# Optimization experiments

Hardware: AMD Instinct MI355X
Metric: run time of the kernel (lower is better)

The kernel has to match this reference:

```python
import jax, jax.numpy as jnp
import numpy as np

B = 512       # batch_size
IN = 256      # input_size
H = 512       # hidden_size
OUT = 64      # output_size
N_PAIRS = B - 1   # number of H0 persistence deaths (connected components merges)
TOL = 1e-6    # rtol for torch.isclose
ATOL = 1e-8   # torch default atol
EPS = 0.0     # homology_eps
TARGET_P = 1.0
HOM_P = 1.0
COMP_P = 0.01

_IU = np.triu_indices(B, 1)  # condensed pdist indexing, static


def _mlp(batch, W1, b1, W2, b2, W3, b3, Wout, bout):
    # FeedForward: input->hidden, (n_layers-1) hidden->hidden, hidden->output, ReLU
    h = jax.nn.relu(batch @ W1 + b1)
    h = jax.nn.relu(h @ W2 + b2)
    h = jax.nn.relu(h @ W3 + b3)
    return h @ Wout + bout


def _pdist(y):
    # condensed euclidean pairwise distances, same ordering as torch F.pdist
    d = y[_IU[0]] - y[_IU[1]]                 # [P, OUT]
    return jnp.sqrt(jnp.sum(d * d, axis=-1))  # [P]


def setup_inputs() -> dict:
    key = jax.random.key(0)
    ks = jax.random.split(key, 8)
    batch = jax.random.normal(ks[0], (B, IN), jnp.float32)
    target = jax.random.normal(ks[1], (B, OUT), jnp.float32)
    W1 = jax.random.normal(ks[2], (IN, H), jnp.float32) / np.sqrt(IN)
    W2 = jax.random.normal(ks[3], (H, H), jnp.float32) / np.sqrt(H)
    W3 = jax.random.normal(ks[4], (H, H), jnp.float32) / np.sqrt(H)
    Wout = jax.random.normal(ks[5], (H, OUT), jnp.float32) / np.sqrt(H)
    b1 = jnp.zeros((H,), jnp.float32)
    b2 = jnp.zeros((H,), jnp.float32)
    b3 = jnp.zeros((H,), jnp.float32)
    bout = jnp.zeros((OUT,), jnp.float32)
    # persistence deaths = actual critical pdist values (from the external
    # Vietoris-Rips routine in the original); sample N_PAIRS distinct entries.
    y0 = _mlp(batch, W1, b1, W2, b2, W3, b3, Wout, bout)
    pd0 = np.asarray(_pdist(y0))
    idx = np.random.default_rng(0).choice(pd0.shape[0], N_PAIRS, replace=False)
    persistence_deaths = jnp.asarray(pd0[idx], jnp.float32)
    return {"batch": batch, "target": target,
            "W1": W1, "b1": b1, "W2": W2, "b2": b2, "W3": W3, "b3": b3,
            "Wout": Wout, "bout": bout,
            "persistence_deaths": persistence_deaths}


def reference(batch, target, W1, b1, W2, b2, W3, b3, Wout, bout, persistence_deaths):
    y = _mlp(batch, W1, b1, W2, b2, W3, b3, Wout, bout)   # [B, OUT]
    y_hom = y  # normalize_for_homology = False
    pd = _pdist(y_hom)                                     # [P]
    # vectorized indicator_death over all pairs (replaces per-pair Python loop)
    mask = jnp.any(jnp.isclose(pd[:, None], persistence_deaths[None, :],
                               rtol=TOL, atol=ATOL), axis=1)      # [P] bool
    # homology_dim=0: birth_pdist = 0; norm=1 of selected (death - 0 + eps)
    homology_loss = jnp.sum(jnp.abs(jnp.where(mask, pd + EPS, 0.0)))
    target_loss = jnp.mean((target - y) ** 2)
    compactness_loss = jnp.sum(jnp.abs(y - jnp.mean(y, axis=0, keepdims=True)))
    loss = TARGET_P * target_loss + HOM_P * homology_loss + COMP_P * compactness_loss
    return loss
```

## Files before the change

kernel.cpp:

```cpp
#include <hip/hip_runtime.h>

#define B_    512
#define IN_   256
#define H_    512
#define OUT_  64
#define NDEATH (B_ - 1)
#define NSORT  512
#define RTOL_ 1e-6
#define ATOL_ 1e-8
#define NBLK  256
#define NTHR  512
#define KT    32

typedef __attribute__((ext_vector_type(4))) double d4_t;

__device__ __forceinline__ void ast(double* p, double v) {
    __hip_atomic_store(p, v, __ATOMIC_RELAXED, __HIP_MEMORY_SCOPE_AGENT);
}
__device__ __forceinline__ double ald(const double* p) {
    return __hip_atomic_load(p, __ATOMIC_RELAXED, __HIP_MEMORY_SCOPE_AGENT);
}

__device__ __forceinline__ void lbar() {
    asm volatile("s_waitcnt lgkmcnt(0)" ::: "memory");
    __builtin_amdgcn_s_barrier();
    asm volatile("" ::: "memory");
}

__device__ __forceinline__ void gbar(unsigned* cnt, unsigned nb) {
    __syncthreads();
    if (threadIdx.x == 0) {
        __hip_atomic_fetch_add(cnt, 1u, __ATOMIC_RELAXED,
                               __HIP_MEMORY_SCOPE_AGENT);
        while (__hip_atomic_load(cnt, __ATOMIC_RELAXED,
                                 __HIP_MEMORY_SCOPE_AGENT) < nb)
            __builtin_amdgcn_s_sleep(2);
    }
    __syncthreads();
}

__device__ void sort_windows(const float* __restrict__ deaths,
                             double* sd, double* slo, double* shi, int t) {
    if (t < NSORT) sd[t] = (t < NDEATH) ? (double)deaths[t] : 1e300;
    __syncthreads();
    for (int k = 2; k <= NSORT; k <<= 1) {
        for (int j = k >> 1; j > 0; j >>= 1) {
            if (t < 256) {
                int l = ((t & ~(j - 1)) << 1) | (t & (j - 1));
                int p = l + j;
                bool up = ((l & k) == 0);
                double a = sd[l], b = sd[p];
                if ((a > b) == up) { sd[l] = b; sd[p] = a; }
            }
            __syncthreads();
        }
    }
    if (t < NSORT) {
        double d = sd[t];
        double w = ATOL_ + RTOL_ * fabs(d);
        slo[t] = d - w;
        shi[t] = d + w;
    }
    __syncthreads();
}

template <typename TIN, bool RELU>
__device__ void gemm_dev(const TIN* __restrict__ A, const float* __restrict__ W,
                         const float* __restrict__ bias, double* __restrict__ C,
                         int N, int K, int tile, int t,
                         double (&As)[2][2][KT][33], double (&Ws)[2][2][KT][33]) {
    const int lane  = t & 63;
    const int wave4 = (t >> 6) & 3;
    const int w2    = t >> 8;
    const int tg    = t & 255;
    const int wm    = wave4 & 1, wn = wave4 >> 1;
    const int nbx   = N >> 5;
    const int row0  = (tile / nbx) << 5;
    const int col0  = (tile % nbx) << 5;

    const int akk   = tg & 31;
    const int amm   = tg >> 5;
    const int wnn   = tg & 31;
    const int wkk   = tg >> 5;
    const int kbase = w2 * (K >> 1);
    const int nkt   = K >> 6;

    TIN   ar[2][4];
    float wr[2][4];

    auto load_to = [&](int rs, int kt) {
        const int k0 = kbase + (kt << 5);
        #pragma unroll
        for (int p = 0; p < 4; ++p) {
            ar[rs][p] = A[(size_t)(row0 + amm + 8 * p) * K + k0 + akk];
            wr[rs][p] = W[(size_t)(k0 + wkk + 8 * p) * N + col0 + wnn];
        }
    };
    auto stage = [&](int rs, int buf) {
        #pragma unroll
        for (int p = 0; p < 4; ++p) {
            As[w2][buf][akk][amm + 8 * p] = (double)ar[rs][p];
            Ws[w2][buf][wkk + 8 * p][wnn] = (double)wr[rs][p];
        }
    };

    load_to(0, 0);
    if (nkt > 1) load_to(1, 1);
    stage(0, 0);
    lbar();

    d4_t c4 = {0.0, 0.0, 0.0, 0.0};
    const int mrow = wm * 16 + (lane & 15);
    const int ncol = wn * 16 + (lane & 15);
    const int kq   = lane >> 4;

    for (int kt = 0; kt < nkt; ++kt) {
        const int cur = kt & 1;
        if (kt + 2 < nkt) load_to(cur, kt + 2);
        #pragma unroll
        for (int ks = 0; ks < KT / 4; ++ks) {
            double av = As[w2][cur][ks * 4 + kq][mrow];
            double bv = Ws[w2][cur][ks * 4 + kq][ncol];
            c4 = __builtin_amdgcn_mfma_f64_16x16x4f64(av, bv, c4, 0, 0, 0);
        }
        if (kt + 1 < nkt) stage(cur ^ 1, cur ^ 1);
        lbar();
    }

    double (*cEx)[16][17] = (double (*)[16][17])(&As[0][0][0][0]);
    const int r4 = (lane >> 4) * 4;
    if (w2 == 1) {
        #pragma unroll
        for (int r = 0; r < 4; ++r)
            cEx[wave4][r4 + r][lane & 15] = c4[r];
    }
    lbar();
    if (w2 == 0) {
        #pragma unroll
        for (int r = 0; r < 4; ++r) {
            int row = row0 + wm * 16 + r4 + r;
            int col = col0 + wn * 16 + (lane & 15);
            double v = c4[r] + cEx[wave4][r4 + r][lane & 15] + (double)bias[col];
            if (RELU) v = v > 0.0 ? v : 0.0;
            ast(&C[(size_t)row * N + col], v);
        }
    }
}

__device__ void mc_dev(const float* __restrict__ target,
                       const double* __restrict__ y,
                       double* __restrict__ t_part, double* __restrict__ c_part,
                       int c, int t) {
    const int wave = t >> 6, lane = t & 63;
    double v = y[(size_t)t * OUT_ + c];
    double s = v;
    for (int off = 32; off; off >>= 1) s += __shfl_down(s, off);
    __shared__ double swm[8];
    __shared__ double smean;
    if (lane == 0) swm[wave] = s;
    __syncthreads();
    if (t == 0) {
        double m = 0.0;
        #pragma unroll
        for (int w = 0; w < 8; ++w) m += swm[w];
        smean = m / (double)B_;
    }
    __syncthreads();
    double m = smean;
    double d = (double)target[(size_t)t * OUT_ + c] - v;
    double t_s = d * d;
    double c_s = fabs(v - m);
    for (int off = 32; off; off >>= 1) {
        t_s += __shfl_down(t_s, off);
        c_s += __shfl_down(c_s, off);
    }
    __shared__ double st[8], sc[8];
    if (lane == 0) { st[wave] = t_s; sc[wave] = c_s; }
    __syncthreads();
    if (t == 0) {
        double ts = 0.0, cs = 0.0;
        #pragma unroll
        for (int w = 0; w < 8; ++w) { ts += st[w]; cs += sc[w]; }
        ast(&t_part[c], ts);
        ast(&c_part[c], cs);
    }
}

__device__ __forceinline__ double pair_val(const double* __restrict__ yrow_s,
                                           const double* __restrict__ yj,
                                           const double* __restrict__ slo,
                                           const double* __restrict__ shi) {
    double s = 0.0;
    #pragma unroll
    for (int d = 0; d < OUT_; d += 2) {
        double2 v = *(const double2*)(yj + d);
        double d0 = yrow_s[d]     - v.x;
        double d1 = yrow_s[d + 1] - v.y;
        s = fma(d0, d0, s);
        s = fma(d1, d1, s);
    }
    double pd = sqrt(s);
    int pos = 0;
    #pragma unroll
    for (int step = NSORT / 2; step; step >>= 1) {
        if (slo[pos + step - 1] <= pd) pos += step;
    }
    bool m = (pos > 0) && (shi[pos - 1] >= pd);
    return m ? pd : 0.0;
}

__device__ void pdist_dev(const double* __restrict__ y,
                          double* __restrict__ hom_part, int bid, int t,
                          double* yA, double* yB,
                          const double* slo, const double* shi) {
    const int iA = bid;
    const int iB = 510 - bid;
    if (t < OUT_)            yA[t]        = y[(size_t)iA * OUT_ + t];
    else if (t < 2 * OUT_)   yB[t - OUT_] = y[(size_t)iB * OUT_ + (t - OUT_)];
    __syncthreads();

    double local = 0.0;
    for (int j = iA + 1 + t; j < B_; j += NTHR)
        local += pair_val(yA, y + (size_t)j * OUT_, slo, shi);
    if (iB != iA)
        for (int j = iB + 1 + t; j < B_; j += NTHR)
            local += pair_val(yB, y + (size_t)j * OUT_, slo, shi);

    for (int off = 32; off; off >>= 1) local += __shfl_down(local, off);
    __shared__ double sw[8];
    int wave = t >> 6, lane = t & 63;
    if (lane == 0) sw[wave] = local;
    __syncthreads();
    if (t == 0) {
        double s = 0.0;
        #pragma unroll
        for (int w = 0; w < 8; ++w) s += sw[w];
        ast(&hom_part[bid], s);
    }
}

__global__ __launch_bounds__(NTHR) void fused_k(
    const float* __restrict__ batch, const float* __restrict__ target,
    const float* __restrict__ W1, const float* __restrict__ b1,
    const float* __restrict__ W2, const float* __restrict__ b2,
    const float* __restrict__ W3, const float* __restrict__ b3,
    const float* __restrict__ Wout, const float* __restrict__ bout,
    const float* __restrict__ deaths, float* __restrict__ out,
    double* __restrict__ hA, double* __restrict__ hB,
    double* __restrict__ hC, double* __restrict__ yv,
    double* __restrict__ hom_part, double* __restrict__ t_part,
    double* __restrict__ c_part, unsigned* __restrict__ cnt,
    double* __restrict__ wbc) {
    const int bid = blockIdx.x;
    const int t   = threadIdx.x;
    const int g   = bid >> 4;
    const int c   = bid & 15;
    unsigned* gc  = cnt + g * 32;

    __shared__ double As[2][2][KT][33];
    __shared__ double Ws[2][2][KT][33];
    __shared__ double slo[NSORT], shi[NSORT];
    __shared__ double yA[OUT_], yB[OUT_];
    __shared__ int    lastf;
    double* sd = &As[0][0][0][0];

    gemm_dev<float,  true>(batch, W1, b1, hA, H_, IN_, bid, t, As, Ws);
    gbar(&gc[0], 16);
    gemm_dev<double, true>(hA, W2, b2, hB, H_, H_, bid, t, As, Ws);
    gbar(&gc[1], 16);
    gemm_dev<double, true>(hB, W3, b3, hC, H_, H_, bid, t, As, Ws);
    gbar(&gc[2], 16);

    if (c < 2) {
        gemm_dev<double, false>(hC, Wout, bout, yv, OUT_, H_, g * 2 + c, t, As, Ws);
    } else {
        sort_windows(deaths, sd, slo, shi, t);
        if (bid == 2 && t < NSORT) {
            ast(&wbc[t],         slo[t]);
            ast(&wbc[NSORT + t], shi[t]);
        }
    }

    gbar(&cnt[512], NBLK);
    if (c < 2) {
        if (t < NSORT) {
            slo[t] = ald(&wbc[t]);
            shi[t] = ald(&wbc[NSORT + t]);
        }
        __syncthreads();
    }

    pdist_dev(yv, hom_part, bid, t, yA, yB, slo, shi);
    if (bid < OUT_) mc_dev(target, yv, t_part, c_part, bid, t);

    __syncthreads();
    if (t == 0) {
        unsigned prev = __hip_atomic_fetch_add(&cnt[544], 1u, __ATOMIC_RELAXED,
                                               __HIP_MEMORY_SCOPE_AGENT);
        lastf = (prev == NBLK - 1);
    }
    __syncthreads();
    if (lastf) {
        double h = 0.0, tp = 0.0, cp = 0.0;
        if (t < NBLK)
            h = __hip_atomic_load(&hom_part[t], __ATOMIC_RELAXED,
                                  __HIP_MEMORY_SCOPE_AGENT);
        if (t < OUT_) {
            tp = __hip_atomic_load(&t_part[t], __ATOMIC_RELAXED,
                                   __HIP_MEMORY_SCOPE_AGENT);
            cp = __hip_atomic_load(&c_part[t], __ATOMIC_RELAXED,
                                   __HIP_MEMORY_SCOPE_AGENT);
        }
        for (int off = 32; off; off >>= 1) {
            h  += __shfl_down(h,  off);
            tp += __shfl_down(tp, off);
            cp += __shfl_down(cp, off);
        }
        __shared__ double sh[8], stp[8], scp[8];
        int wave = t >> 6, lane = t & 63;
        if (lane == 0) { sh[wave] = h; stp[wave] = tp; scp[wave] = cp; }
        __syncthreads();
        if (t == 0) {
            double hs = 0.0, ts = 0.0, cs = 0.0;
            #pragma unroll
            for (int w = 0; w < 8; ++w) {
                hs += sh[w]; ts += stp[w]; cs += scp[w];
            }
            out[0] = (float)(ts / (double)(B_ * OUT_) + hs + 0.01 * cs);
        }
    }
}

extern "C" void kernel_launch(void* const* d_in, const int* in_sizes, int n_in,
                              void* d_out, int out_size, void* d_ws, size_t ws_size,
                              hipStream_t stream) {
    const float* batch  = (const float*)d_in[0];
    const float* target = (const float*)d_in[1];
    const float* W1     = (const float*)d_in[2];
    const float* b1     = (const float*)d_in[3];
    const float* W2     = (const float*)d_in[4];
    const float* b2     = (const float*)d_in[5];
    const float* W3     = (const float*)d_in[6];
    const float* b3     = (const float*)d_in[7];
    const float* Wout   = (const float*)d_in[8];
    const float* bout   = (const float*)d_in[9];
    const float* deaths = (const float*)d_in[10];
    float* out = (float*)d_out;

    double* hA       = (double*)d_ws;
    double* hB       = hA + (size_t)B_ * H_;
    double* hC       = hB + (size_t)B_ * H_;
    double* yv       = hC + (size_t)B_ * H_;
    double* hom_part = yv + (size_t)B_ * OUT_;
    double* t_part   = hom_part + NBLK;
    double* c_part   = t_part + OUT_;
    unsigned* cnt    = (unsigned*)(c_part + OUT_);
    double* wbc      = (double*)(cnt + 576);

    hipMemsetAsync(cnt, 0, 576 * sizeof(unsigned), stream);

    fused_k<<<dim3(NBLK), dim3(NTHR), 0, stream>>>(
        batch, target, W1, b1, W2, b2, W3, b3, Wout, bout, deaths, out,
        hA, hB, hC, yv, hom_part, t_part, c_part, cnt, wbc);
}
```

Measured before the change: 130.0 us.

## Load GEMM B operands directly to registers and use hierarchical grid barriers

The GEMM no longer stages the weight tile in shared memory. Each lane loads its B fragment straight from global memory into registers, with a three-deep register prefetch, and the accumulation is split into two independent MFMA chains. The final all-block barrier and the last-block reduction become two-level trees: group leaders gather their 16 blocks, then block 0 waits on the root counter. The barrier poll sleep is also shortened. This cuts LDS traffic and atomic contention, at the cost of more register pressure and strided, less coalesced global loads of W.

```diff
diff --git a/kernel.cpp b/kernel.cpp
--- a/kernel.cpp
+++ b/kernel.cpp
@@ -20,6 +20,12 @@
 __device__ __forceinline__ double ald(const double* p) {
     return __hip_atomic_load(p, __ATOMIC_RELAXED, __HIP_MEMORY_SCOPE_AGENT);
 }
+__device__ __forceinline__ unsigned aldu(const unsigned* p) {
+    return __hip_atomic_load(p, __ATOMIC_RELAXED, __HIP_MEMORY_SCOPE_AGENT);
+}
+__device__ __forceinline__ void aadd(unsigned* p) {
+    __hip_atomic_fetch_add(p, 1u, __ATOMIC_RELAXED, __HIP_MEMORY_SCOPE_AGENT);
+}
 
 __device__ __forceinline__ void lbar() {
     asm volatile("s_waitcnt lgkmcnt(0)" ::: "memory");
@@ -30,11 +36,22 @@
 __device__ __forceinline__ void gbar(unsigned* cnt, unsigned nb) {
     __syncthreads();
     if (threadIdx.x == 0) {
-        __hip_atomic_fetch_add(cnt, 1u, __ATOMIC_RELAXED,
-                               __HIP_MEMORY_SCOPE_AGENT);
-        while (__hip_atomic_load(cnt, __ATOMIC_RELAXED,
-                                 __HIP_MEMORY_SCOPE_AGENT) < nb)
-            __builtin_amdgcn_s_sleep(2);
+        aadd(cnt);
+        while (aldu(cnt) < nb) __builtin_amdgcn_s_sleep(1);
+    }
+    __syncthreads();
+}
+
+__device__ __forceinline__ void gbar2(unsigned* gslot, unsigned* root,
+                                      int leader) {
+    __syncthreads();
+    if (threadIdx.x == 0) {
+        aadd(gslot);
+        if (leader) {
+            while (aldu(gslot) < 16u) __builtin_amdgcn_s_sleep(1);
+            aadd(root);
+        }
+        while (aldu(root) < 16u) __builtin_amdgcn_s_sleep(1);
     }
     __syncthreads();
 }
@@ -68,7 +85,7 @@
 __device__ void gemm_dev(const TIN* __restrict__ A, const float* __restrict__ W,
                          const float* __restrict__ bias, double* __restrict__ C,
                          int N, int K, int tile, int t,
-                         double (&As)[2][2][KT][33], double (&Ws)[2][2][KT][33]) {
+                         double (&As)[2][2][KT][33]) {
     const int lane  = t & 63;
     const int wave4 = (t >> 6) & 3;
     const int w2    = t >> 8;
@@ -80,52 +97,65 @@
 
     const int akk   = tg & 31;
     const int amm   = tg >> 5;
-    const int wnn   = tg & 31;
-    const int wkk   = tg >> 5;
     const int kbase = w2 * (K >> 1);
     const int nkt   = K >> 6;
 
-    TIN   ar[2][4];
-    float wr[2][4];
-
-    auto load_to = [&](int rs, int kt) {
+    const int mrow  = wm * 16 + (lane & 15);
+    const int ncol  = wn * 16 + (lane & 15);
+    const int kq    = lane >> 4;
+
+    TIN   ar[3][4];
+    float br[3][8];
+
+    auto load_a = [&](int rs, int kt) {
         const int k0 = kbase + (kt << 5);
         #pragma unroll
-        for (int p = 0; p < 4; ++p) {
+        for (int p = 0; p < 4; ++p)
             ar[rs][p] = A[(size_t)(row0 + amm + 8 * p) * K + k0 + akk];
-            wr[rs][p] = W[(size_t)(k0 + wkk + 8 * p) * N + col0 + wnn];
-        }
     };
-    auto stage = [&](int rs, int buf) {
-        #pragma unroll
-        for (int p = 0; p < 4; ++p) {
+    auto load_b = [&](int rs, int kt) {
+        const int k0 = kbase + (kt << 5);
+        const float* wp = W + (size_t)(k0 + kq) * N + col0 + ncol;
+        #pragma unroll
+        for (int ks = 0; ks < 8; ++ks)
+            br[rs][ks] = wp[(size_t)(4 * ks) * N];
+    };
+    auto stage_a = [&](int rs, int buf) {
+        #pragma unroll
+        for (int p = 0; p < 4; ++p)
             As[w2][buf][akk][amm + 8 * p] = (double)ar[rs][p];
-            Ws[w2][buf][wkk + 8 * p][wnn] = (double)wr[rs][p];
-        }
     };
 
-    load_to(0, 0);
-    if (nkt > 1) load_to(1, 1);
-    stage(0, 0);
+    load_a(0, 0); load_b(0, 0);
+    if (nkt > 1) { load_a(1, 1); load_b(1, 1); }
+    if (nkt > 2) { load_a(2, 2); load_b(2, 2); }
+    stage_a(0, 0);
     lbar();
 
-    d4_t c4 = {0.0, 0.0, 0.0, 0.0};
-    const int mrow = wm * 16 + (lane & 15);
-    const int ncol = wn * 16 + (lane & 15);
-    const int kq   = lane >> 4;
+    d4_t c4a = {0.0, 0.0, 0.0, 0.0};
+    d4_t c4b = {0.0, 0.0, 0.0, 0.0};
 
     for (int kt = 0; kt < nkt; ++kt) {
         const int cur = kt & 1;
-        if (kt + 2 < nkt) load_to(cur, kt + 2);
-        #pragma unroll
-        for (int ks = 0; ks < KT / 4; ++ks) {
+        const int rs  = kt % 3;
+        #pragma unroll
+        for (int ks = 0; ks < 4; ++ks) {
             double av = As[w2][cur][ks * 4 + kq][mrow];
-            double bv = Ws[w2][cur][ks * 4 + kq][ncol];
-            c4 = __builtin_amdgcn_mfma_f64_16x16x4f64(av, bv, c4, 0, 0, 0);
-        }
-        if (kt + 1 < nkt) stage(cur ^ 1, cur ^ 1);
+            c4a = __builtin_amdgcn_mfma_f64_16x16x4f64(av, (double)br[rs][ks],
+                                                       c4a, 0, 0, 0);
+        }
+        #pragma unroll
+        for (int ks = 4; ks < 8; ++ks) {
+            double av = As[w2][cur][ks * 4 + kq][mrow];
+            c4b = __builtin_amdgcn_mfma_f64_16x16x4f64(av, (double)br[rs][ks],
+                                                       c4b, 0, 0, 0);
+        }
+        if (kt + 3 < nkt) { load_a(rs, kt + 3); load_b(rs, kt + 3); }
+        if (kt + 1 < nkt) stage_a((kt + 1) % 3, cur ^ 1);
         lbar();
     }
+
+    d4_t c4 = c4a + c4b;
 
     double (*cEx)[16][17] = (double (*)[16][17])(&As[0][0][0][0]);
     const int r4 = (lane >> 4) * 4;
@@ -258,21 +288,19 @@
     unsigned* gc  = cnt + g * 32;
 
     __shared__ double As[2][2][KT][33];
-    __shared__ double Ws[2][2][KT][33];
     __shared__ double slo[NSORT], shi[NSORT];
     __shared__ double yA[OUT_], yB[OUT_];
-    __shared__ int    lastf;
     double* sd = &As[0][0][0][0];
 
-    gemm_dev<float,  true>(batch, W1, b1, hA, H_, IN_, bid, t, As, Ws);
+    gemm_dev<float,  true>(batch, W1, b1, hA, H_, IN_, bid, t, As);
     gbar(&gc[0], 16);
-    gemm_dev<double, true>(hA, W2, b2, hB, H_, H_, bid, t, As, Ws);
+    gemm_dev<double, true>(hA, W2, b2, hB, H_, H_, bid, t, As);
     gbar(&gc[1], 16);
-    gemm_dev<double, true>(hB, W3, b3, hC, H_, H_, bid, t, As, Ws);
+    gemm_dev<double, true>(hB, W3, b3, hC, H_, H_, bid, t, As);
     gbar(&gc[2], 16);
 
     if (c < 2) {
-        gemm_dev<double, false>(hC, Wout, bout, yv, OUT_, H_, g * 2 + c, t, As, Ws);
+        gemm_dev<double, false>(hC, Wout, bout, yv, OUT_, H_, g * 2 + c, t, As);
     } else {
         sort_windows(deaths, sd, slo, shi, t);
         if (bid == 2 && t < NSORT) {
@@ -281,7 +309,7 @@
         }
     }
 
-    gbar(&cnt[512], NBLK);
+    gbar2(&gc[3], &cnt[512], c == 0);
     if (c < 2) {
         if (t < NSORT) {
             slo[t] = ald(&wbc[t]);
@@ -295,22 +323,21 @@
 
     __syncthreads();
     if (t == 0) {
-        unsigned prev = __hip_atomic_fetch_add(&cnt[544], 1u, __ATOMIC_RELAXED,
-                                               __HIP_MEMORY_SCOPE_AGENT);
-        lastf = (prev == NBLK - 1);
-    }
-    __syncthreads();
-    if (lastf) {
+        aadd(&gc[4]);
+        if (c == 0) {
+            while (aldu(&gc[4]) < 16u) __builtin_amdgcn_s_sleep(1);
+            aadd(&cnt[513]);
+        }
+    }
+    if (bid != 0) return;
+    if (t == 0)
+        while (aldu(&cnt[513]) < 16u) __builtin_amdgcn_s_sleep(1);
+    __syncthreads();
+
+    {
         double h = 0.0, tp = 0.0, cp = 0.0;
-        if (t < NBLK)
-            h = __hip_atomic_load(&hom_part[t], __ATOMIC_RELAXED,
-                                  __HIP_MEMORY_SCOPE_AGENT);
-        if (t < OUT_) {
-            tp = __hip_atomic_load(&t_part[t], __ATOMIC_RELAXED,
-                                   __HIP_MEMORY_SCOPE_AGENT);
-            cp = __hip_atomic_load(&c_part[t], __ATOMIC_RELAXED,
-                                   __HIP_MEMORY_SCOPE_AGENT);
-        }
+        if (t < NBLK) h = ald(&hom_part[t]);
+        if (t < OUT_) { tp = ald(&t_part[t]); cp = ald(&c_part[t]); }
         for (int off = 32; off; off >>= 1) {
             h  += __shfl_down(h,  off);
             tp += __shfl_down(tp, off);
```

Result: faster. 122.3 us (-5.9%).
